# Optimization experiments

Measured on AMD Instinct MI355X. Metric: run time of the kernel, lower is better.

The kernel has to match this reference:

```python
import jax, jax.numpy as jnp
import numpy as np

W_REG = 3.0
N_CAND = 4
IOU_LEN = 15.0
BIG_COST = 1e8


def focal_cost(cls_pred, gt_labels, alpha=0.25, gamma=2.0, eps=1e-12):
    # cls_pred: [B,P,C] logits, gt_labels: [B,T] int -> [B,P,T]
    p = jax.nn.sigmoid(cls_pred)
    neg = -jnp.log(1.0 - p + eps) * (1.0 - alpha) * p ** gamma
    pos = -jnp.log(p + eps) * alpha * (1.0 - p) ** gamma
    B, P, _ = cls_pred.shape
    T = gt_labels.shape[1]
    idx = jnp.broadcast_to(gt_labels[:, None, :], (B, P, T))
    return jnp.take_along_axis(pos, idx, axis=2) - jnp.take_along_axis(neg, idx, axis=2)


def line_iou(pred, target, img_w, length=IOU_LEN):
    # pred: [B,P,O], target: [B,T,O] -> [B,P,T] (unaligned)
    px1, px2 = pred - length, pred + length
    tx1, tx2 = target - length, target + length
    ovr = jnp.minimum(px2[:, :, None, :], tx2[:, None, :, :]) - jnp.maximum(px1[:, :, None, :], tx1[:, None, :, :])
    union = jnp.maximum(px2[:, :, None, :], tx2[:, None, :, :]) - jnp.minimum(px1[:, :, None, :], tx1[:, None, :, :])
    invalid = ((target < 0) | (target >= img_w))[:, None, :, :]
    ovr = jnp.where(invalid, 0.0, ovr)
    union = jnp.where(invalid, 0.0, union)
    return ovr.sum(-1) / (union.sum(-1) + 1e-9)


def clrnet_assign(preds, targets, masks, img_w, img_h):
    B, P, _ = preds.shape
    T = targets.shape[1]
    w = float(img_w - 1)
    h = float(img_h - 1)
    pa = preds.at[..., 3].multiply(w).at[..., 6:].multiply(w)
    ta = targets.at[..., 3].multiply(w).at[..., 6:].multiply(w)
    p_off, t_off = pa[..., 6:], ta[..., 6:]

    # --- distance score (masked mean L1 over valid target x-offsets) ---
    tvalid = (t_off >= 0) & (t_off < img_w)                      # [B,T,O]
    cmask = tvalid[:, None, :, :]                                 # [B,1,T,O]
    clen = jnp.maximum(cmask.sum(-1).astype(pa.dtype), 1.0)      # [B,1,T]
    diff = jnp.abs(p_off[:, :, None, :] - t_off[:, None, :, :]) * cmask  # [B,P,T,O]
    distances = diff.sum(-1) / clen                               # [B,P,T]
    dist_max = jnp.maximum(distances.max(axis=(1, 2), keepdims=True), 1e-8)
    dist_score = 1.0 - distances / dist_max + 0.01

    # --- start-point score (euclidean on (y*(h), x)) ---
    ps = pa[..., 2:4].at[..., 0].multiply(h)
    ts = ta[..., 2:4].at[..., 0].multiply(h)
    start_d = jnp.sqrt(((ps[:, :, None, :] - ts[:, None, :, :]) ** 2).sum(-1))
    start_max = jnp.maximum(start_d.max(axis=(1, 2), keepdims=True), 1e-8)
    start_score = 1.0 - start_d / start_max + 0.01

    # --- theta score ---
    th_d = jnp.abs(pa[..., 4][:, :, None] - ta[..., 4][:, None, :]) * 180.0
    th_max = jnp.maximum(th_d.max(axis=(1, 2), keepdims=True), 1e-8)
    th_score = 1.0 - th_d / th_max + 0.01

    # --- total cost ---
    gt_labels = ta[..., 1].astype(jnp.int32)
    cls_cost = focal_cost(pa[..., :2], gt_labels)
    reg = (jnp.maximum(dist_score, 1e-3) * jnp.maximum(start_score, 1e-3)
           * jnp.maximum(th_score, 1e-3))
    total_cost = -(reg ** 2) * W_REG + cls_cost                   # [B,P,T]
    valid_t = (masks > 0)[:, None, :]                             # [B,1,T]
    total_cost = jnp.where(valid_t, total_cost, BIG_COST)

    # --- dynamic-k from line IoU ---
    liou = jnp.nan_to_num(line_iou(p_off, t_off, img_w), nan=0.0)
    liou = jnp.where(valid_t, liou, 0.0)
    k = min(N_CAND, P)
    topk_ious, _ = jax.lax.top_k(jnp.swapaxes(liou, 1, 2), k)     # [B,T,k]
    dynamic_ks = jnp.maximum(topk_ious.sum(-1).astype(jnp.int32), 1)
    dynamic_ks = jnp.where(masks > 0, dynamic_ks, 0)              # [B,T]

    # --- top-k lowest-cost priors per target, scatter into matching matrix ---
    _, topk_idx = jax.lax.top_k(-jnp.swapaxes(total_cost, 1, 2), k)  # [B,T,k]
    sel = (jnp.arange(k)[None, None, :] < dynamic_ks[:, :, None]).astype(total_cost.dtype)  # [B,T,k]
    one_hot_p = jax.nn.one_hot(topk_idx, P, dtype=total_cost.dtype)  # [B,T,k,P]
    matching = jnp.swapaxes((one_hot_p * sel[..., None]).sum(2), 1, 2)  # [B,P,T]

    # --- conflict resolution: a prior matched to >1 targets keeps argmin-cost one ---
    conflict = matching.sum(-1) > 1                               # [B,P]
    masked_cost = jnp.where(matching == 0, jnp.inf, total_cost)
    best_t = jnp.argmin(masked_cost, axis=2)                      # [B,P]
    new_m = jax.nn.one_hot(best_t, T, dtype=matching.dtype)
    matching = jnp.where(conflict[..., None], new_m, matching)

    has_match = matching.sum(-1) > 0.5
    t_idx = jnp.argmax(matching, axis=2)
    matched = jnp.where(has_match, t_idx, -1).astype(jnp.int32)
    return matched >= 0, matched


def setup_inputs() -> dict:
    key = jax.random.key(0)
    k1, k2, k3 = jax.random.split(key, 3)
    B, P, T, O = 32, 1000, 16, 72
    D = 6 + O
    preds = jax.random.uniform(k1, (B, P, D), dtype=jnp.float32)
    # slightly outside [0,1] so the invalid-offset masking path is exercised
    targets = jax.random.uniform(k2, (B, T, D), dtype=jnp.float32, minval=-0.05, maxval=1.05)
    masks = jax.random.randint(k3, (B, T), 0, 2).astype(jnp.int32)
    return {"preds": preds, "targets": targets, "masks": masks, "img_w": 800, "img_h": 320}


def reference(preds, targets, masks, img_w, img_h):
    return clrnet_assign(preds, targets, masks, img_w, img_h)
```

## Files before the change

kernel.cpp:

```cpp
#include <hip/hip_runtime.h>
#include <math.h>

#define B_ 32
#define P_ 1000
#define T_ 16
#define D_ 78
#define O_ 72
#define NXB 16
#define BIGC 100000000.0f

__global__ __launch_bounds__(256) void k1(
        const float* __restrict__ preds, const float* __restrict__ targets,
        const int* __restrict__ imgw_p, const int* __restrict__ imgh_p,
        float* __restrict__ dist, float* __restrict__ liou,
        float4* __restrict__ scal4, float* __restrict__ pths,
        float* __restrict__ pmax) {
    __shared__ float pred_s[64 * 81];
    __shared__ float2 tomg[T_ * O_];
    __shared__ float cnt_s[T_], clen_s[T_], ts0_s[T_], ts1_s[T_], tth_s[T_];
    __shared__ float red[256];

    const int b = blockIdx.y, bx = blockIdx.x;
    const int p0 = bx * 64;
    const int rows = min(64, P_ - p0);
    const float w = (float)(imgw_p[0] - 1);
    const float h = (float)(imgh_p[0] - 1);
    const float imgwf = (float)imgw_p[0];

    {
        const float4* gbase = (const float4*)(preds + ((size_t)b * P_ + p0) * D_);
        const int n4 = rows * D_ / 4;
        for (int i = threadIdx.x; i < n4; i += 256) {
            float4 v = gbase[i];
            int base = i * 4;
            int r = base / D_, c = base - r * D_;
#pragma unroll
            for (int k = 0; k < 4; ++k) {
                int cc = c + k, rr = r;
                if (cc >= D_) { cc -= D_; ++rr; }
                float x = (&v.x)[k];
                if (cc >= 6 || cc == 3) x *= w;
                pred_s[rr * 81 + cc] = x;
            }
        }
    }
    for (int i = threadIdx.x; i < T_ * O_; i += 256) {
        int t = i / O_, o = i - t * O_;
        float to = targets[((size_t)b * T_ + t) * D_ + 6 + o] * w;
        float m = (to >= 0.f && to < imgwf) ? 1.f : 0.f;
        tomg[((t >> 2) * O_ + o) * 4 + (t & 3)] = make_float2(to, m);
    }
    __syncthreads();
    if (threadIdx.x < T_) {
        int t = threadIdx.x;
        float c = 0.f;
        for (int o = 0; o < O_; ++o) c += tomg[((t >> 2) * O_ + o) * 4 + (t & 3)].y;
        cnt_s[t] = c;
        clen_s[t] = fmaxf(c, 1.f);
        const float* tr = targets + ((size_t)b * T_ + t) * D_;
        ts0_s[t] = tr[2] * h;
        ts1_s[t] = tr[3] * w;
        tth_s[t] = tr[4];
    }
    __syncthreads();

    const int lane = threadIdx.x & 63;
    const int g = threadIdx.x >> 6;
    const int p = p0 + lane;

    float ldm = 0.f, lsm = 0.f, ltm = 0.f;
    if (p < P_) {
        const float* lrow = pred_s + lane * 81;
        float S0 = 0.f, S1 = 0.f, S2 = 0.f, S3 = 0.f;
        const float4* tg4 = (const float4*)(tomg + (size_t)g * O_ * 4);
#pragma unroll 4
        for (int o = 0; o < O_; ++o) {
            float po = lrow[6 + o];
            float4 r0 = tg4[2 * o];
            float4 r1 = tg4[2 * o + 1];
            S0 += r0.y * fabsf(po - r0.x);
            S1 += r0.w * fabsf(po - r0.z);
            S2 += r1.y * fabsf(po - r1.x);
            S3 += r1.w * fabsf(po - r1.z);
        }
        float Sv[4] = {S0, S1, S2, S3};
        float ps0 = lrow[2] * h, ps1 = lrow[3], pth = lrow[4];
#pragma unroll
        for (int j = 0; j < 4; ++j) {
            int t = 4 * g + j;
            float dv = Sv[j] / clen_s[t];
            dist[(size_t)(b * T_ + t) * P_ + p] = dv;
            ldm = fmaxf(ldm, dv);
            float c30 = 30.f * cnt_s[t];
            liou[(size_t)(b * T_ + t) * P_ + p] = (c30 - Sv[j]) / (c30 + Sv[j] + 1e-9f);
            float d0 = ps0 - ts0_s[t], d1 = ps1 - ts1_s[t];
            lsm = fmaxf(lsm, sqrtf(d0 * d0 + d1 * d1));
            ltm = fmaxf(ltm, fabsf(pth - tth_s[t]) * 180.f);
        }
        if (g == 0) {
            float fc[2];
#pragma unroll
            for (int c = 0; c < 2; ++c) {
                float x = lrow[c];
                float pc = 1.f / (1.f + expf(-x));
                float neg = -logf(1.f - pc + 1e-12f) * 0.75f * pc * pc;
                float pos = -logf(pc + 1e-12f) * 0.25f * (1.f - pc) * (1.f - pc);
                fc[c] = pos - neg;
            }
            scal4[(size_t)b * P_ + p] = make_float4(fc[0], fc[1], ps0, ps1);
            pths[(size_t)b * P_ + p] = pth;
        }
    }

    red[threadIdx.x] = ldm; __syncthreads();
    for (int s = 128; s; s >>= 1) {
        if (threadIdx.x < s) red[threadIdx.x] = fmaxf(red[threadIdx.x], red[threadIdx.x + s]);
        __syncthreads();
    }
    float m0 = red[0]; __syncthreads();
    red[threadIdx.x] = lsm; __syncthreads();
    for (int s = 128; s; s >>= 1) {
        if (threadIdx.x < s) red[threadIdx.x] = fmaxf(red[threadIdx.x], red[threadIdx.x + s]);
        __syncthreads();
    }
    float m1 = red[0]; __syncthreads();
    red[threadIdx.x] = ltm; __syncthreads();
    for (int s = 128; s; s >>= 1) {
        if (threadIdx.x < s) red[threadIdx.x] = fmaxf(red[threadIdx.x], red[threadIdx.x + s]);
        __syncthreads();
    }
    if (threadIdx.x == 0) {
        float* q = pmax + (size_t)(b * NXB + bx) * 3;
        q[0] = m0; q[1] = m1; q[2] = red[0];
    }
}

__global__ __launch_bounds__(256) void k2(
        const float* __restrict__ targets, const int* __restrict__ masks,
        const int* __restrict__ imgw_p, const int* __restrict__ imgh_p,
        const float* __restrict__ dist, const float* __restrict__ liou,
        const float4* __restrict__ scal4, const float* __restrict__ pths,
        const float* __restrict__ pmax,
        float* __restrict__ cost, int4* __restrict__ sel) {
    const int wid = blockIdx.x * 4 + (threadIdx.x >> 6);
    const int lane = threadIdx.x & 63;
    if (wid >= B_ * T_) return;
    const int b = wid >> 4, t = wid & 15;

    float dm = 0.f, sm = 0.f, tm = 0.f;
    for (int i = 0; i < NXB; ++i) {
        const float* q = pmax + (size_t)(b * NXB + i) * 3;
        dm = fmaxf(dm, q[0]); sm = fmaxf(sm, q[1]); tm = fmaxf(tm, q[2]);
    }
    dm = fmaxf(dm, 1e-8f); sm = fmaxf(sm, 1e-8f); tm = fmaxf(tm, 1e-8f);

    const float w = (float)(imgw_p[0] - 1);
    const float h = (float)(imgh_p[0] - 1);
    const float* tr = targets + (size_t)(b * T_ + t) * D_;
    const float ts0 = tr[2] * h, ts1 = tr[3] * w, tth = tr[4];
    int lab = (int)tr[1]; lab = lab < 0 ? 0 : (lab > 1 ? 1 : lab);
    const int mk = masks[b * T_ + t];

    const float* drow = dist + (size_t)(b * T_ + t) * P_;
    const float* lrow = liou + (size_t)(b * T_ + t) * P_;
    float* crow = cost + (size_t)(b * T_ + t) * P_;
    const float4* s4b = scal4 + (size_t)b * P_;
    const float* ptb = pths + (size_t)b * P_;

    float lv[16], cv[16];
#pragma unroll
    for (int i = 0; i < 16; ++i) {
        int p = lane + 64 * i;
        if (p < P_) {
            float d = drow[p];
            float4 s4 = s4b[p];
            float pth = ptb[p];
            float dsc = 1.f - d / dm + 0.01f;
            float d0 = s4.z - ts0, d1 = s4.w - ts1;
            float ssc = 1.f - sqrtf(d0 * d0 + d1 * d1) / sm + 0.01f;
            float tsc = 1.f - fabsf(pth - tth) * 180.f / tm + 0.01f;
            float reg = fmaxf(dsc, 1e-3f) * fmaxf(ssc, 1e-3f) * fmaxf(tsc, 1e-3f);
            float c = -(reg * reg) * 3.f + (lab ? s4.y : s4.x);
            if (mk <= 0) c = BIGC;
            crow[p] = c;
            cv[i] = c;
            lv[i] = lrow[p];
        } else {
            cv[i] = INFINITY;
            lv[i] = -INFINITY;
        }
    }

    float sum = 0.f;
    for (int r = 0; r < 4; ++r) {
        float bv = -INFINITY; int bi = 0x7fffffff;
#pragma unroll
        for (int i = 0; i < 16; ++i) {
            if (lv[i] > bv) { bv = lv[i]; bi = lane + 64 * i; }
        }
        for (int off = 32; off; off >>= 1) {
            float ov = __shfl_xor(bv, off, 64);
            int oi = __shfl_xor(bi, off, 64);
            if (ov > bv || (ov == bv && oi < bi)) { bv = ov; bi = oi; }
        }
        sum += bv;
        if ((bi & 63) == lane) lv[bi >> 6] = -INFINITY;
    }
    int dk = 0;
    if (mk > 0) {
        dk = (int)sum;
        if (dk < 1) dk = 1;
        if (dk > 4) dk = 4;
    }

    int selp[4];
#pragma unroll
    for (int r = 0; r < 4; ++r) {
        float bv = INFINITY; int bi = 0x7fffffff;
#pragma unroll
        for (int i = 0; i < 16; ++i) {
            if (cv[i] < bv) { bv = cv[i]; bi = lane + 64 * i; }
        }
        for (int off = 32; off; off >>= 1) {
            float ov = __shfl_xor(bv, off, 64);
            int oi = __shfl_xor(bi, off, 64);
            if (ov < bv || (ov == bv && oi < bi)) { bv = ov; bi = oi; }
        }
        selp[r] = bi;
        if ((bi & 63) == lane) cv[bi >> 6] = INFINITY;
    }

    if (lane == 0) {
        sel[wid] = make_int4(dk > 0 ? selp[0] : -1, dk > 1 ? selp[1] : -1,
                             dk > 2 ? selp[2] : -1, dk > 3 ? selp[3] : -1);
    }
}

__global__ __launch_bounds__(256) void k3(const int4* __restrict__ sel,
                                          const float* __restrict__ cost,
                                          int* __restrict__ out) {
    __shared__ int selE[64];
    const int b = blockIdx.x;
    if (threadIdx.x < 64) selE[threadIdx.x] = ((const int*)sel)[b * 64 + threadIdx.x];
    __syncthreads();

#pragma unroll
    for (int k = 0; k < 4; ++k) {
        int p = k * 256 + threadIdx.x;
        if (p >= P_) continue;
        unsigned int m = 0;
#pragma unroll
        for (int t = 0; t < T_; ++t) {
            bool hit = (selE[4 * t] == p) | (selE[4 * t + 1] == p) |
                       (selE[4 * t + 2] == p) | (selE[4 * t + 3] == p);
            if (hit) m |= 1u << t;
        }
        int matched = -1;
        if (m) {
            if (__popc(m) == 1) {
                matched = __ffs(m) - 1;
            } else {
                float best = INFINITY;
#pragma unroll
                for (int t = 0; t < T_; ++t) {
                    if ((m >> t) & 1u) {
                        float c = cost[(size_t)(b * T_ + t) * P_ + p];
                        if (c < best) { best = c; matched = t; }
                    }
                }
            }
        }
        out[b * P_ + p] = (matched >= 0) ? 1 : 0;
        out[B_ * P_ + b * P_ + p] = matched;
    }
}

extern "C" void kernel_launch(void* const* d_in, const int* in_sizes, int n_in,
                              void* d_out, int out_size, void* d_ws, size_t ws_size,
                              hipStream_t stream) {
    const float* preds   = (const float*)d_in[0];
    const float* targets = (const float*)d_in[1];
    const int*   masks   = (const int*)d_in[2];
    const int*   imgw    = (const int*)d_in[3];
    const int*   imgh    = (const int*)d_in[4];
    int* out = (int*)d_out;

    char* ws = (char*)d_ws;
    const size_t SZ = (size_t)B_ * T_ * P_ * sizeof(float);
    float*  dist  = (float*)ws;
    float*  liou  = (float*)(ws + SZ);
    float*  cost  = (float*)(ws + 2 * SZ);
    float4* scal4 = (float4*)(ws + 3 * SZ);
    float*  pths  = (float*)(ws + 3 * SZ + (size_t)B_ * P_ * 16);
    float*  pmax  = (float*)(ws + 3 * SZ + (size_t)B_ * P_ * 20);
    int4*   sel   = (int4*)(ws + 3 * SZ + (size_t)B_ * P_ * 20 + (size_t)B_ * NXB * 3 * 4 + 64);

    k1<<<dim3(NXB, B_), 256, 0, stream>>>(preds, targets, imgw, imgh, dist, liou, scal4, pths, pmax);
    k2<<<128, 256, 0, stream>>>(targets, masks, imgw, imgh, dist, liou, scal4, pths, pmax, cost, sel);
    k3<<<B_, 256, 0, stream>>>(sel, cost, out);
}
```

Before: 37.39 us.

## Assign one block per (batch,target) pair in k2 with two-level top-k reduction

The cost/top-k kernel now uses a full 256-thread block per (b,t) pair instead of one wavefront, so each thread handles 4 priors instead of 16. Each wave computes its local top-4 for IoU and cost via shuffles, writes them to shared memory, and thread 0 merges the 16 candidates per list. This raises parallelism and shortens per-thread serial top-k loops, at the cost of a block barrier and a serial merge on one thread.

Result: slower. 40.34 us (+7.9%).

```diff
diff --git a/kernel.cpp b/kernel.cpp
--- a/kernel.cpp
+++ b/kernel.cpp
@@ -142,10 +142,13 @@
         const float4* __restrict__ scal4, const float* __restrict__ pths,
         const float* __restrict__ pmax,
         float* __restrict__ cost, int4* __restrict__ sel) {
-    const int wid = blockIdx.x * 4 + (threadIdx.x >> 6);
-    const int lane = threadIdx.x & 63;
-    if (wid >= B_ * T_) return;
+    __shared__ float lval[4][4], cval[4][4];
+    __shared__ int lidx[4][4], cidx[4][4];
+
+    const int wid = blockIdx.x;
     const int b = wid >> 4, t = wid & 15;
+    const int tid = threadIdx.x;
+    const int wv = tid >> 6;
 
     float dm = 0.f, sm = 0.f, tm = 0.f;
     for (int i = 0; i < NXB; ++i) {
@@ -167,10 +170,10 @@
     const float4* s4b = scal4 + (size_t)b * P_;
     const float* ptb = pths + (size_t)b * P_;
 
-    float lv[16], cv[16];
-#pragma unroll
-    for (int i = 0; i < 16; ++i) {
-        int p = lane + 64 * i;
+    float lv[4], cv[4];
+#pragma unroll
+    for (int i = 0; i < 4; ++i) {
+        int p = tid + 256 * i;
         if (p < P_) {
             float d = drow[p];
             float4 s4 = s4b[p];
@@ -191,46 +194,69 @@
         }
     }
 
-    float sum = 0.f;
     for (int r = 0; r < 4; ++r) {
         float bv = -INFINITY; int bi = 0x7fffffff;
 #pragma unroll
-        for (int i = 0; i < 16; ++i) {
-            if (lv[i] > bv) { bv = lv[i]; bi = lane + 64 * i; }
+        for (int i = 0; i < 4; ++i) {
+            if (lv[i] > bv) { bv = lv[i]; bi = tid + 256 * i; }
         }
         for (int off = 32; off; off >>= 1) {
             float ov = __shfl_xor(bv, off, 64);
             int oi = __shfl_xor(bi, off, 64);
             if (ov > bv || (ov == bv && oi < bi)) { bv = ov; bi = oi; }
         }
-        sum += bv;
-        if ((bi & 63) == lane) lv[bi >> 6] = -INFINITY;
-    }
-    int dk = 0;
-    if (mk > 0) {
-        dk = (int)sum;
-        if (dk < 1) dk = 1;
-        if (dk > 4) dk = 4;
-    }
-
-    int selp[4];
-#pragma unroll
+        if ((tid & 63) == 0) { lval[wv][r] = bv; lidx[wv][r] = bi; }
+        if ((bi & 255) == tid) lv[bi >> 8] = -INFINITY;
+    }
     for (int r = 0; r < 4; ++r) {
         float bv = INFINITY; int bi = 0x7fffffff;
 #pragma unroll
-        for (int i = 0; i < 16; ++i) {
-            if (cv[i] < bv) { bv = cv[i]; bi = lane + 64 * i; }
+        for (int i = 0; i < 4; ++i) {
+            if (cv[i] < bv) { bv = cv[i]; bi = tid + 256 * i; }
         }
         for (int off = 32; off; off >>= 1) {
             float ov = __shfl_xor(bv, off, 64);
             int oi = __shfl_xor(bi, off, 64);
             if (ov < bv || (ov == bv && oi < bi)) { bv = ov; bi = oi; }
         }
-        selp[r] = bi;
-        if ((bi & 63) == lane) cv[bi >> 6] = INFINITY;
-    }
-
-    if (lane == 0) {
+        if ((tid & 63) == 0) { cval[wv][r] = bv; cidx[wv][r] = bi; }
+        if ((bi & 255) == tid) cv[bi >> 8] = INFINITY;
+    }
+    __syncthreads();
+
+    if (tid == 0) {
+        float sum = 0.f;
+        unsigned int used = 0;
+        for (int r = 0; r < 4; ++r) {
+            float bv = -INFINITY; int bi = 0x7fffffff, bj = -1;
+#pragma unroll
+            for (int j = 0; j < 16; ++j) {
+                if (used & (1u << j)) continue;
+                float v = lval[j >> 2][j & 3]; int ix = lidx[j >> 2][j & 3];
+                if (v > bv || (v == bv && ix < bi)) { bv = v; bi = ix; bj = j; }
+            }
+            used |= 1u << bj;
+            sum += bv;
+        }
+        int dk = 0;
+        if (mk > 0) {
+            dk = (int)sum;
+            if (dk < 1) dk = 1;
+            if (dk > 4) dk = 4;
+        }
+        int selp[4];
+        used = 0;
+        for (int r = 0; r < 4; ++r) {
+            float bv = INFINITY; int bi = 0x7fffffff, bj = -1;
+#pragma unroll
+            for (int j = 0; j < 16; ++j) {
+                if (used & (1u << j)) continue;
+                float v = cval[j >> 2][j & 3]; int ix = cidx[j >> 2][j & 3];
+                if (v < bv || (v == bv && ix < bi)) { bv = v; bi = ix; bj = j; }
+            }
+            used |= 1u << bj;
+            selp[r] = bi;
+        }
         sel[wid] = make_int4(dk > 0 ? selp[0] : -1, dk > 1 ? selp[1] : -1,
                              dk > 2 ? selp[2] : -1, dk > 3 ? selp[3] : -1);
     }
@@ -296,6 +322,6 @@
     int4*   sel   = (int4*)(ws + 3 * SZ + (size_t)B_ * P_ * 20 + (size_t)B_ * NXB * 3 * 4 + 64);
 
     k1<<<dim3(NXB, B_), 256, 0, stream>>>(preds, targets, imgw, imgh, dist, liou, scal4, pths, pmax);
-    k2<<<128, 256, 0, stream>>>(targets, masks, imgw, imgh, dist, liou, scal4, pths, pmax, cost, sel);
+    k2<<<B_ * T_, 256, 0, stream>>>(targets, masks, imgw, imgh, dist, liou, scal4, pths, pmax, cost, sel);
     k3<<<B_, 256, 0, stream>>>(sel, cost, out);
 }
```

## Fuse selection and conflict kernels, widen k1 to 1024 threads with split-O reduction

Applied to the files above, without the earlier changes.

k2 and k3 merge into one kernel with one 1024-thread block per batch. The 16 waves each handle one target and write their top-k picks to shared memory, and the same block then resolves conflicts. This removes one launch and the global sel round trip. k1 now uses 1024 threads that split the 72 offsets into four quarters, combines the partial sums through shared memory, and replaces the tree reductions with wave shuffles. In exchange, k2 runs only 32 blocks, which lowers parallelism for the cost and top-k phase.

Result: no change. 37.60 us (+0.6%).

```diff
diff --git a/kernel.cpp b/kernel.cpp
--- a/kernel.cpp
+++ b/kernel.cpp
@@ -9,7 +9,7 @@
 #define NXB 16
 #define BIGC 100000000.0f
 
-__global__ __launch_bounds__(256) void k1(
+__global__ __launch_bounds__(1024, 8) void k1(
         const float* __restrict__ preds, const float* __restrict__ targets,
         const int* __restrict__ imgw_p, const int* __restrict__ imgh_p,
         float* __restrict__ dist, float* __restrict__ liou,
@@ -17,12 +17,14 @@
         float* __restrict__ pmax) {
     __shared__ float pred_s[64 * 81];
     __shared__ float2 tomg[T_ * O_];
+    __shared__ float Spart[T_][4][64];
+    __shared__ float wmax[16][3];
     __shared__ float cnt_s[T_], clen_s[T_], ts0_s[T_], ts1_s[T_], tth_s[T_];
-    __shared__ float red[256];
 
     const int b = blockIdx.y, bx = blockIdx.x;
     const int p0 = bx * 64;
     const int rows = min(64, P_ - p0);
+    const int tid = threadIdx.x;
     const float w = (float)(imgw_p[0] - 1);
     const float h = (float)(imgh_p[0] - 1);
     const float imgwf = (float)imgw_p[0];
@@ -30,7 +32,7 @@
     {
         const float4* gbase = (const float4*)(preds + ((size_t)b * P_ + p0) * D_);
         const int n4 = rows * D_ / 4;
-        for (int i = threadIdx.x; i < n4; i += 256) {
+        for (int i = tid; i < n4; i += 1024) {
             float4 v = gbase[i];
             int base = i * 4;
             int r = base / D_, c = base - r * D_;
@@ -44,15 +46,15 @@
             }
         }
     }
-    for (int i = threadIdx.x; i < T_ * O_; i += 256) {
+    for (int i = tid; i < T_ * O_; i += 1024) {
         int t = i / O_, o = i - t * O_;
         float to = targets[((size_t)b * T_ + t) * D_ + 6 + o] * w;
         float m = (to >= 0.f && to < imgwf) ? 1.f : 0.f;
         tomg[((t >> 2) * O_ + o) * 4 + (t & 3)] = make_float2(to, m);
     }
     __syncthreads();
-    if (threadIdx.x < T_) {
-        int t = threadIdx.x;
+    if (tid < T_) {
+        int t = tid;
         float c = 0.f;
         for (int o = 0; o < O_; ++o) c += tomg[((t >> 2) * O_ + o) * 4 + (t & 3)].y;
         cnt_s[t] = c;
@@ -64,17 +66,18 @@
     }
     __syncthreads();
 
-    const int lane = threadIdx.x & 63;
-    const int g = threadIdx.x >> 6;
-    const int p = p0 + lane;
-
-    float ldm = 0.f, lsm = 0.f, ltm = 0.f;
-    if (p < P_) {
+    {
+        const int lane = tid & 63;
+        const int wv = tid >> 6;
+        const int tg = wv & 3;
+        const int oq = wv >> 2;
         const float* lrow = pred_s + lane * 81;
+        const float4* tg4 = (const float4*)(tomg + (size_t)tg * O_ * 4);
+        const int o_lo = oq * 18;
         float S0 = 0.f, S1 = 0.f, S2 = 0.f, S3 = 0.f;
-        const float4* tg4 = (const float4*)(tomg + (size_t)g * O_ * 4);
-#pragma unroll 4
-        for (int o = 0; o < O_; ++o) {
+#pragma unroll
+        for (int i = 0; i < 18; ++i) {
+            int o = o_lo + i;
             float po = lrow[6 + o];
             float4 r0 = tg4[2 * o];
             float4 r1 = tg4[2 * o + 1];
@@ -83,25 +86,33 @@
             S2 += r1.y * fabsf(po - r1.x);
             S3 += r1.w * fabsf(po - r1.z);
         }
-        float Sv[4] = {S0, S1, S2, S3};
-        float ps0 = lrow[2] * h, ps1 = lrow[3], pth = lrow[4];
-#pragma unroll
-        for (int j = 0; j < 4; ++j) {
-            int t = 4 * g + j;
-            float dv = Sv[j] / clen_s[t];
-            dist[(size_t)(b * T_ + t) * P_ + p] = dv;
-            ldm = fmaxf(ldm, dv);
-            float c30 = 30.f * cnt_s[t];
-            liou[(size_t)(b * T_ + t) * P_ + p] = (c30 - Sv[j]) / (c30 + Sv[j] + 1e-9f);
-            float d0 = ps0 - ts0_s[t], d1 = ps1 - ts1_s[t];
-            lsm = fmaxf(lsm, sqrtf(d0 * d0 + d1 * d1));
-            ltm = fmaxf(ltm, fabsf(pth - tth_s[t]) * 180.f);
-        }
-        if (g == 0) {
+        Spart[4 * tg + 0][oq][lane] = S0;
+        Spart[4 * tg + 1][oq][lane] = S1;
+        Spart[4 * tg + 2][oq][lane] = S2;
+        Spart[4 * tg + 3][oq][lane] = S3;
+    }
+    __syncthreads();
+
+    const int th = tid >> 6, pl = tid & 63;
+    const int p = p0 + pl;
+    float ldm = 0.f, lsm = 0.f, ltm = 0.f;
+    if (pl < rows) {
+        float S = ((Spart[th][0][pl] + Spart[th][1][pl]) + Spart[th][2][pl]) + Spart[th][3][pl];
+        float dv = S / clen_s[th];
+        dist[(size_t)(b * T_ + th) * P_ + p] = dv;
+        ldm = dv;
+        float c30 = 30.f * cnt_s[th];
+        liou[(size_t)(b * T_ + th) * P_ + p] = (c30 - S) / (c30 + S + 1e-9f);
+        const float* prow = pred_s + pl * 81;
+        float ps0 = prow[2] * h, ps1 = prow[3], pth = prow[4];
+        float d0 = ps0 - ts0_s[th], d1 = ps1 - ts1_s[th];
+        lsm = sqrtf(d0 * d0 + d1 * d1);
+        ltm = fabsf(pth - tth_s[th]) * 180.f;
+        if (th == 0) {
             float fc[2];
 #pragma unroll
             for (int c = 0; c < 2; ++c) {
-                float x = lrow[c];
+                float x = prow[c];
                 float pc = 1.f / (1.f + expf(-x));
                 float neg = -logf(1.f - pc + 1e-12f) * 0.75f * pc * pc;
                 float pos = -logf(pc + 1e-12f) * 0.25f * (1.f - pc) * (1.f - pc);
@@ -112,40 +123,39 @@
         }
     }
 
-    red[threadIdx.x] = ldm; __syncthreads();
-    for (int s = 128; s; s >>= 1) {
-        if (threadIdx.x < s) red[threadIdx.x] = fmaxf(red[threadIdx.x], red[threadIdx.x + s]);
-        __syncthreads();
-    }
-    float m0 = red[0]; __syncthreads();
-    red[threadIdx.x] = lsm; __syncthreads();
-    for (int s = 128; s; s >>= 1) {
-        if (threadIdx.x < s) red[threadIdx.x] = fmaxf(red[threadIdx.x], red[threadIdx.x + s]);
-        __syncthreads();
-    }
-    float m1 = red[0]; __syncthreads();
-    red[threadIdx.x] = ltm; __syncthreads();
-    for (int s = 128; s; s >>= 1) {
-        if (threadIdx.x < s) red[threadIdx.x] = fmaxf(red[threadIdx.x], red[threadIdx.x + s]);
-        __syncthreads();
-    }
-    if (threadIdx.x == 0) {
+    for (int off = 32; off; off >>= 1) {
+        ldm = fmaxf(ldm, __shfl_xor(ldm, off, 64));
+        lsm = fmaxf(lsm, __shfl_xor(lsm, off, 64));
+        ltm = fmaxf(ltm, __shfl_xor(ltm, off, 64));
+    }
+    if (pl == 0) { wmax[th][0] = ldm; wmax[th][1] = lsm; wmax[th][2] = ltm; }
+    __syncthreads();
+    if (tid == 0) {
+        float m0 = 0.f, m1 = 0.f, m2 = 0.f;
+#pragma unroll
+        for (int i = 0; i < 16; ++i) {
+            m0 = fmaxf(m0, wmax[i][0]);
+            m1 = fmaxf(m1, wmax[i][1]);
+            m2 = fmaxf(m2, wmax[i][2]);
+        }
         float* q = pmax + (size_t)(b * NXB + bx) * 3;
-        q[0] = m0; q[1] = m1; q[2] = red[0];
+        q[0] = m0; q[1] = m1; q[2] = m2;
     }
 }
 
-__global__ __launch_bounds__(256) void k2(
+__global__ __launch_bounds__(1024) void k2(
         const float* __restrict__ targets, const int* __restrict__ masks,
         const int* __restrict__ imgw_p, const int* __restrict__ imgh_p,
         const float* __restrict__ dist, const float* __restrict__ liou,
         const float4* __restrict__ scal4, const float* __restrict__ pths,
         const float* __restrict__ pmax,
-        float* __restrict__ cost, int4* __restrict__ sel) {
-    const int wid = blockIdx.x * 4 + (threadIdx.x >> 6);
-    const int lane = threadIdx.x & 63;
-    if (wid >= B_ * T_) return;
-    const int b = wid >> 4, t = wid & 15;
+        float* __restrict__ cost, int* __restrict__ out) {
+    __shared__ int selE[64];
+
+    const int b = blockIdx.x;
+    const int tid = threadIdx.x;
+    const int t = tid >> 6;
+    const int lane = tid & 63;
 
     float dm = 0.f, sm = 0.f, tm = 0.f;
     for (int i = 0; i < NXB; ++i) {
@@ -231,29 +241,19 @@
     }
 
     if (lane == 0) {
-        sel[wid] = make_int4(dk > 0 ? selp[0] : -1, dk > 1 ? selp[1] : -1,
-                             dk > 2 ? selp[2] : -1, dk > 3 ? selp[3] : -1);
-    }
-}
-
-__global__ __launch_bounds__(256) void k3(const int4* __restrict__ sel,
-                                          const float* __restrict__ cost,
-                                          int* __restrict__ out) {
-    __shared__ int selE[64];
-    const int b = blockIdx.x;
-    if (threadIdx.x < 64) selE[threadIdx.x] = ((const int*)sel)[b * 64 + threadIdx.x];
-    __syncthreads();
-
-#pragma unroll
-    for (int k = 0; k < 4; ++k) {
-        int p = k * 256 + threadIdx.x;
-        if (p >= P_) continue;
+#pragma unroll
+        for (int j = 0; j < 4; ++j) selE[4 * t + j] = (j < dk) ? selp[j] : -1;
+    }
+    __syncthreads();
+
+    if (tid < P_) {
+        const int p = tid;
         unsigned int m = 0;
 #pragma unroll
-        for (int t = 0; t < T_; ++t) {
-            bool hit = (selE[4 * t] == p) | (selE[4 * t + 1] == p) |
-                       (selE[4 * t + 2] == p) | (selE[4 * t + 3] == p);
-            if (hit) m |= 1u << t;
+        for (int t2 = 0; t2 < T_; ++t2) {
+            bool hit = (selE[4 * t2] == p) | (selE[4 * t2 + 1] == p) |
+                       (selE[4 * t2 + 2] == p) | (selE[4 * t2 + 3] == p);
+            if (hit) m |= 1u << t2;
         }
         int matched = -1;
         if (m) {
@@ -262,10 +262,10 @@
             } else {
                 float best = INFINITY;
 #pragma unroll
-                for (int t = 0; t < T_; ++t) {
-                    if ((m >> t) & 1u) {
-                        float c = cost[(size_t)(b * T_ + t) * P_ + p];
-                        if (c < best) { best = c; matched = t; }
+                for (int t2 = 0; t2 < T_; ++t2) {
+                    if ((m >> t2) & 1u) {
+                        float c = cost[(size_t)(b * T_ + t2) * P_ + p];
+                        if (c < best) { best = c; matched = t2; }
                     }
                 }
             }
@@ -293,9 +293,7 @@
     float4* scal4 = (float4*)(ws + 3 * SZ);
     float*  pths  = (float*)(ws + 3 * SZ + (size_t)B_ * P_ * 16);
     float*  pmax  = (float*)(ws + 3 * SZ + (size_t)B_ * P_ * 20);
-    int4*   sel   = (int4*)(ws + 3 * SZ + (size_t)B_ * P_ * 20 + (size_t)B_ * NXB * 3 * 4 + 64);
-
-    k1<<<dim3(NXB, B_), 256, 0, stream>>>(preds, targets, imgw, imgh, dist, liou, scal4, pths, pmax);
-    k2<<<128, 256, 0, stream>>>(targets, masks, imgw, imgh, dist, liou, scal4, pths, pmax, cost, sel);
-    k3<<<B_, 256, 0, stream>>>(sel, cost, out);
+
+    k1<<<dim3(NXB, B_), 1024, 0, stream>>>(preds, targets, imgw, imgh, dist, liou, scal4, pths, pmax);
+    k2<<<B_, 1024, 0, stream>>>(targets, masks, imgw, imgh, dist, liou, scal4, pths, pmax, cost, out);
 }
```
